# Kernel tuning notes

Measured on AMD Instinct MI355X. Metric: run time of the kernel, lower is better.

## Reference

```python
import jax, jax.numpy as jnp
import numpy as np

P = 8.0  # Lp exponent of the distance neuron (finite-p stage of l_inf-dist training)


def _patches(t, k, stride, pad):
    # [B, Cin, H, W] -> [B, Cin*k*k, H', W'], feature dim ordered channel-major
    return jax.lax.conv_general_dilated_patches(
        t, (k, k), (stride, stride), [(pad, pad), (pad, pad)])


def _lp(d):
    # d: [B, Cout, Cin*k*k, H', W'] nonnegative -> Lp norm over patch dim
    return jnp.power(jnp.sum(jnp.power(d, P), axis=2), 1.0 / P)


def norm_dist_conv(x, l, u, w, stride, pad):
    # Lp-distance "convolution": y[b,o,i,j] = || patch(x)[b,:,i,j] - w[o,:] ||_p
    # mean_normalize=True: zero-center each output unit's weight vector
    Cout, Cin, k, _ = w.shape
    wf = w.reshape(Cout, -1)
    wf = wf - jnp.mean(wf, axis=1, keepdims=True)
    wb = wf[None, :, :, None, None]                      # [1, Cout, Ckk, 1, 1]
    px = _patches(x, k, stride, pad)[:, None]            # [B, 1, Ckk, H', W']
    pl = _patches(l, k, stride, pad)[:, None]
    pu = _patches(u, k, stride, pad)[:, None]
    y = _lp(jnp.abs(px - wb))
    # interval bounds of |x_j - w_j| given x_j in [l_j, u_j], then monotone Lp
    dl = jnp.maximum(jnp.maximum(pl - wb, wb - pu), 0.0)
    du = jnp.maximum(jnp.abs(pl - wb), jnp.abs(pu - wb))
    return y, _lp(dl), _lp(du)


def bound_relu(x, l, u):
    # ReLU is monotone: apply elementwise to value and both bounds
    return jax.nn.relu(x), jax.nn.relu(l), jax.nn.relu(u)


def setup_inputs() -> dict:
    key = jax.random.key(0)
    k1, k2, k3 = jax.random.split(key, 3)
    B, C, H, W = 4, 32, 32, 32
    eps = 0.1  # l_inf perturbation radius
    x = jax.random.normal(k1, (B, C, H, W), dtype=jnp.float32)
    lower = x - eps
    upper = x + eps
    scale = 1.0 / np.sqrt(C * 9)
    weight1 = jax.random.normal(k2, (C, C, 3, 3), dtype=jnp.float32) * scale
    weight2 = jax.random.normal(k3, (C, C, 3, 3), dtype=jnp.float32) * scale
    return {"x": x, "lower": lower, "upper": upper,
            "weight1": weight1, "weight2": weight2}


def reference(x, lower, upper, weight1, weight2):
    # conv1 (stride=1, pad=1) -> BoundReLU -> conv2 -> residual add -> BoundReLU
    o = norm_dist_conv(x, lower, upper, weight1, 1, 1)
    o = bound_relu(*o)
    o = norm_dist_conv(*o, weight2, 1, 1)
    out = (o[0] + x, o[1] + lower, o[2] + upper)  # identity shortcut (stride=1, in==out)
    out = bound_relu(*out)
    return jnp.stack(out)  # [3, B, C, H, W]: (value, lower, upper)
```

## Files before the change

kernel.cpp:

```cpp
#include <hip/hip_runtime.h>

#define NB 4
#define NC 32
#define NH 32
#define NW 32
#define KK 288
#define PLANE (NB*NC*NH*NW)
#define CQ 8
#define SROW 36
#define SPL  (3*SROW)
#define SCH  (6*SPL)
#define STOT (CQ*SCH)

typedef float v2f __attribute__((ext_vector_type(2)));

__device__ __forceinline__ float s3(float v) { return sqrtf(sqrtf(sqrtf(v))); }
__device__ __forceinline__ v2f pkfma(v2f a, v2f b, v2f c) { return __builtin_elementwise_fma(a, b, c); }
__device__ __forceinline__ v2f pkmax(v2f a, v2f b) { return __builtin_elementwise_max(a, b); }

__global__ __launch_bounds__(256) void prep_weights_k(
        const float* __restrict__ w1, const float* __restrict__ w2,
        float* __restrict__ wf1, float* __restrict__ wf2)
{
    const int row = blockIdx.x;
    const float* src = (row < NC) ? w1 : w2;
    float* dst = (row < NC) ? wf1 : wf2;
    const int co = row & (NC - 1);
    const int tid = threadIdx.x;
    __shared__ float red[256];
    const float a = src[co*KK + tid];
    const float b = (tid + 256 < KK) ? src[co*KK + tid + 256] : 0.0f;
    red[tid] = a + b;
    __syncthreads();
    for (int s = 128; s > 0; s >>= 1) {
        if (tid < s) red[tid] += red[tid + s];
        __syncthreads();
    }
    const float mean = red[0] * (1.0f / (float)KK);
    const int q    = ((co >> 4) << 3) | (co & 7);
    const int slot = (co >> 3) & 1;
    {
        const int e = tid, c = e / 9, r9 = e - c*9, r = r9 / 3, kw = r9 - r*3;
        dst[((q*NC + c)*3 + r)*8 + kw*2 + slot] = a - mean;
    }
    if (tid + 256 < KK) {
        const int e = tid + 256, c = e / 9, r9 = e - c*9, r = r9 / 3, kw = r9 - r*3;
        dst[((q*NC + c)*3 + r)*8 + kw*2 + slot] = b - mean;
    }
}

template<bool STAGE2>
__global__ __launch_bounds__(256, 2) void normdist_conv_k(
    const float* __restrict__ sy,
    const float* __restrict__ sl,
    const float* __restrict__ su,
    const float* __restrict__ wf,
    float* __restrict__ pY, float* __restrict__ pL, float* __restrict__ pU)
{
    const int h4   = blockIdx.x;
    const int qg   = blockIdx.y >> 2;
    const int cq   = blockIdx.y & 3;
    const int cq0  = cq * CQ;
    const int b    = blockIdx.z;
    const int tid  = threadIdx.x;
    const int wv   = tid >> 6;
    const int lane = tid & 63;
    const int rsel = lane >> 4;
    const int pp   = lane & 15;
    const int p0   = pp * 2;

    __shared__ float sS[STOT];

    for (int i = tid; i < STOT; i += 256) {
        const int c   = i / SCH;
        int rem       = i - c*SCH;
        const int r   = rem / SPL;
        rem          -= r*SPL;
        const int pl  = rem / SROW;
        const int j   = rem - pl*SROW;
        const int gh  = 4*h4 + r - 1;
        const int gw  = j - 1;
        float v = 0.0f;
        if ((unsigned)gh < NH && (unsigned)gw < NW) {
            const int g = ((b*NC + cq0 + c)*NH + gh)*NW + gw;
            const float* s = (pl == 0) ? sy : (pl == 1) ? sl : su;
            if (STAGE2) {
                v = s3(s[g] + s[PLANE + g] + s[2*PLANE + g] + s[3*PLANE + g]);
            } else {
                v = s[g];
            }
        }
        sS[i] = v;
    }
    __syncthreads();

    const int q = qg*4 + wv;
    const float4* wq = (const float4*)wf + (q*NC + cq0)*6;
    const float* base = &sS[rsel*SPL + p0];

    v2f aY0 = {0,0}, aL0 = {0,0}, aU0 = {0,0};
    v2f aY1 = {0,0}, aL1 = {0,0}, aU1 = {0,0};

    auto tap2 = [&](v2f w, float pxv, float plv, float puv, v2f& aY, v2f& aL, v2f& aU) {
        const v2f P = {pxv, pxv};
        const v2f Lo = {plv, plv};
        const v2f Up = {puv, puv};
        const v2f d  = P - w;
        const v2f d2 = d*d, d4 = d2*d2;
        aY = pkfma(d4, d4, aY);
        const v2f a  = Lo - w;
        const v2f nb = w - Up;
        const v2f z  = {0.0f, 0.0f};
        const v2f m  = pkmax(pkmax(a, nb), z);
        const v2f m2 = m*m, m4 = m2*m2;
        aL = pkfma(m4, m4, aL);
        const v2f a2 = a*a, q2 = nb*nb;
        const v2f mm2 = pkmax(a2, q2);
        const v2f mm4 = mm2*mm2;
        aU = pkfma(mm4, mm4, aU);
    };

    float4 c0 = wq[0], c1 = wq[1], c2 = wq[2], c3 = wq[3], c4 = wq[4], c5 = wq[5];

    for (int c = 0; c < CQ; ++c) {
        const int cn = (c < CQ-1) ? c + 1 : c;
        const float4 n0 = wq[cn*6+0], n1 = wq[cn*6+1], n2 = wq[cn*6+2];
        const float4 n3 = wq[cn*6+3], n4 = wq[cn*6+4], n5 = wq[cn*6+5];

        const float* pb = base + c*SCH;
        #pragma unroll
        for (int dr = 0; dr < 3; ++dr) {
            const float* rb = pb + dr*SPL;
            const float X0 = rb[0],        X1 = rb[1],        X2 = rb[2],        X3 = rb[3];
            const float L0 = rb[SROW+0],   L1 = rb[SROW+1],   L2 = rb[SROW+2],   L3 = rb[SROW+3];
            const float U0 = rb[2*SROW+0], U1 = rb[2*SROW+1], U2 = rb[2*SROW+2], U3 = rb[2*SROW+3];

            const float4 wlo = (dr == 0) ? c0 : (dr == 1) ? c2 : c4;
            const float4 whi = (dr == 0) ? c1 : (dr == 1) ? c3 : c5;
            const v2f w0 = {wlo.x, wlo.y};
            const v2f w1 = {wlo.z, wlo.w};
            const v2f w2 = {whi.x, whi.y};

            tap2(w0, X0, L0, U0, aY0, aL0, aU0);
            tap2(w1, X1, L1, U1, aY0, aL0, aU0);
            tap2(w2, X2, L2, U2, aY0, aL0, aU0);
            tap2(w0, X1, L1, U1, aY1, aL1, aU1);
            tap2(w1, X2, L2, U2, aY1, aL1, aU1);
            tap2(w2, X3, L3, U3, aY1, aL1, aU1);
        }

        c0 = n0; c1 = n1; c2 = n2; c3 = n3; c4 = n4; c5 = n5;
    }

    const int co0 = ((q >> 3) << 4) | (q & 7);
    const int h   = 4*h4 + rsel;
    const int o   = ((b*NC + co0)*NH + h)*NW + p0;
    const int o1  = o + 8*NH*NW;

    float* dY = pY + cq*PLANE;
    float* dL = pL + cq*PLANE;
    float* dU = pU + cq*PLANE;
    *(float2*)&dY[o]  = make_float2(aY0.x, aY1.x);
    *(float2*)&dY[o1] = make_float2(aY0.y, aY1.y);
    *(float2*)&dL[o]  = make_float2(aL0.x, aL1.x);
    *(float2*)&dL[o1] = make_float2(aL0.y, aL1.y);
    *(float2*)&dU[o]  = make_float2(aU0.x, aU1.x);
    *(float2*)&dU[o1] = make_float2(aU0.y, aU1.y);
}

__global__ __launch_bounds__(256) void epilogue_k(
    const float* __restrict__ pY, const float* __restrict__ pL, const float* __restrict__ pU,
    const float* __restrict__ x,  const float* __restrict__ l,  const float* __restrict__ u,
    float* __restrict__ out)
{
    const int i = blockIdx.x*256 + threadIdx.x;
    const float4* pY4 = (const float4*)pY;
    const float4* pL4 = (const float4*)pL;
    const float4* pU4 = (const float4*)pU;
    const float4* x4  = (const float4*)x;
    const float4* l4  = (const float4*)l;
    const float4* u4  = (const float4*)u;
    float4* out4 = (float4*)out;
    const int Q = PLANE/4;

    const float4 ya = pY4[i], yb = pY4[Q+i], yc = pY4[2*Q+i], yd = pY4[3*Q+i];
    const float4 la = pL4[i], lb = pL4[Q+i], lc = pL4[2*Q+i], ld = pL4[3*Q+i];
    const float4 ua = pU4[i], ub = pU4[Q+i], uc = pU4[2*Q+i], ud = pU4[3*Q+i];
    const float4 xr = x4[i], lr = l4[i], ur = u4[i];

    float4 oy, ol, ou;
    oy.x = fmaxf(s3(ya.x+yb.x+yc.x+yd.x) + xr.x, 0.0f);
    oy.y = fmaxf(s3(ya.y+yb.y+yc.y+yd.y) + xr.y, 0.0f);
    oy.z = fmaxf(s3(ya.z+yb.z+yc.z+yd.z) + xr.z, 0.0f);
    oy.w = fmaxf(s3(ya.w+yb.w+yc.w+yd.w) + xr.w, 0.0f);
    ol.x = fmaxf(s3(la.x+lb.x+lc.x+ld.x) + lr.x, 0.0f);
    ol.y = fmaxf(s3(la.y+lb.y+lc.y+ld.y) + lr.y, 0.0f);
    ol.z = fmaxf(s3(la.z+lb.z+lc.z+ld.z) + lr.z, 0.0f);
    ol.w = fmaxf(s3(la.w+lb.w+lc.w+ld.w) + lr.w, 0.0f);
    ou.x = fmaxf(s3(ua.x+ub.x+uc.x+ud.x) + ur.x, 0.0f);
    ou.y = fmaxf(s3(ua.y+ub.y+uc.y+ud.y) + ur.y, 0.0f);
    ou.z = fmaxf(s3(ua.z+ub.z+uc.z+ud.z) + ur.z, 0.0f);
    ou.w = fmaxf(s3(ua.w+ub.w+uc.w+ud.w) + ur.w, 0.0f);

    out4[i]       = oy;
    out4[Q + i]   = ol;
    out4[2*Q + i] = ou;
}

extern "C" void kernel_launch(void* const* d_in, const int* in_sizes, int n_in,
                              void* d_out, int out_size, void* d_ws, size_t ws_size,
                              hipStream_t stream)
{
    const float* x  = (const float*)d_in[0];
    const float* l  = (const float*)d_in[1];
    const float* u  = (const float*)d_in[2];
    const float* w1 = (const float*)d_in[3];
    const float* w2 = (const float*)d_in[4];
    float* ws  = (float*)d_ws;
    float* wf1 = ws;
    float* wf2 = wf1 + 12288;
    float* p1Y = wf2 + 12288;
    float* p1L = p1Y + 4*PLANE;
    float* p1U = p1L + 4*PLANE;
    float* p2Y = p1U + 4*PLANE;
    float* p2L = p2Y + 4*PLANE;
    float* p2U = p2L + 4*PLANE;
    float* out = (float*)d_out;

    prep_weights_k<<<64, 256, 0, stream>>>(w1, w2, wf1, wf2);

    dim3 grd(NH/4, 16, NB);
    normdist_conv_k<false><<<grd, 256, 0, stream>>>(x, l, u, wf1, p1Y, p1L, p1U);
    normdist_conv_k<true ><<<grd, 256, 0, stream>>>(p1Y, p1L, p1U, wf2, p2Y, p2L, p2U);
    epilogue_k<<<PLANE/1024, 256, 0, stream>>>(p2Y, p2L, p2U, x, l, u, out);
}
```

Baseline: 115.0 us.

## Retile conv blocks to one row per block with interleaved float4 shared tile

Each block now covers a single output row and all 16 weight-pair groups for one channel quarter, instead of four rows and four weight groups. The shared tile stores x, lower and upper interleaved as float4, so each tap needs one LDS read instead of three. Input staging per block shrinks to three rows, halo overhead per output rises, and the register prefetch of the next channel's weights is dropped. Each lane now reads different weights (q depends on ps), so weight loads are less uniform across the wavefront.

```diff
diff --git a/kernel.cpp b/kernel.cpp
--- a/kernel.cpp
+++ b/kernel.cpp
@@ -7,10 +7,6 @@
 #define KK 288
 #define PLANE (NB*NC*NH*NW)
 #define CQ 8
-#define SROW 36
-#define SPL  (3*SROW)
-#define SCH  (6*SPL)
-#define STOT (CQ*SCH)
 
 typedef float v2f __attribute__((ext_vector_type(2)));
 
@@ -57,54 +53,51 @@
     const float* __restrict__ wf,
     float* __restrict__ pY, float* __restrict__ pL, float* __restrict__ pU)
 {
-    const int h4   = blockIdx.x;
-    const int qg   = blockIdx.y >> 2;
-    const int cq   = blockIdx.y & 3;
+    const int h    = blockIdx.x;
+    const int cq   = blockIdx.y;
     const int cq0  = cq * CQ;
     const int b    = blockIdx.z;
     const int tid  = threadIdx.x;
     const int wv   = tid >> 6;
     const int lane = tid & 63;
-    const int rsel = lane >> 4;
+    const int ps   = lane >> 4;
     const int pp   = lane & 15;
     const int p0   = pp * 2;
 
-    __shared__ float sS[STOT];
-
-    for (int i = tid; i < STOT; i += 256) {
-        const int c   = i / SCH;
-        int rem       = i - c*SCH;
-        const int r   = rem / SPL;
-        rem          -= r*SPL;
-        const int pl  = rem / SROW;
-        const int j   = rem - pl*SROW;
-        const int gh  = 4*h4 + r - 1;
-        const int gw  = j - 1;
-        float v = 0.0f;
+    __shared__ float4 sP[CQ*3*34];
+
+    for (int i = tid; i < CQ*3*34; i += 256) {
+        const int c   = i / 102;
+        const int rem = i - c*102;
+        const int r   = rem / 34;
+        const int col = rem - r*34;
+        const int gh  = h + r - 1;
+        const int gw  = col - 1;
+        float vx = 0.0f, vl = 0.0f, vu = 0.0f;
         if ((unsigned)gh < NH && (unsigned)gw < NW) {
             const int g = ((b*NC + cq0 + c)*NH + gh)*NW + gw;
-            const float* s = (pl == 0) ? sy : (pl == 1) ? sl : su;
             if (STAGE2) {
-                v = s3(s[g] + s[PLANE + g] + s[2*PLANE + g] + s[3*PLANE + g]);
+                vx = s3(sy[g] + sy[PLANE + g] + sy[2*PLANE + g] + sy[3*PLANE + g]);
+                vl = s3(sl[g] + sl[PLANE + g] + sl[2*PLANE + g] + sl[3*PLANE + g]);
+                vu = s3(su[g] + su[PLANE + g] + su[2*PLANE + g] + su[3*PLANE + g]);
             } else {
-                v = s[g];
+                vx = sy[g]; vl = sl[g]; vu = su[g];
             }
         }
-        sS[i] = v;
+        sP[i] = make_float4(vx, vl, vu, 0.0f);
     }
     __syncthreads();
 
-    const int q = qg*4 + wv;
+    const int q = wv*4 + ps;
     const float4* wq = (const float4*)wf + (q*NC + cq0)*6;
-    const float* base = &sS[rsel*SPL + p0];
 
     v2f aY0 = {0,0}, aL0 = {0,0}, aU0 = {0,0};
     v2f aY1 = {0,0}, aL1 = {0,0}, aU1 = {0,0};
 
-    auto tap2 = [&](v2f w, float pxv, float plv, float puv, v2f& aY, v2f& aL, v2f& aU) {
-        const v2f P = {pxv, pxv};
-        const v2f Lo = {plv, plv};
-        const v2f Up = {puv, puv};
+    auto tap2 = [&](v2f w, const float4& p, v2f& aY, v2f& aL, v2f& aU) {
+        const v2f P  = {p.x, p.x};
+        const v2f Lo = {p.y, p.y};
+        const v2f Up = {p.z, p.z};
         const v2f d  = P - w;
         const v2f d2 = d*d, d4 = d2*d2;
         aY = pkfma(d4, d4, aY);
@@ -120,40 +113,29 @@
         aU = pkfma(mm4, mm4, aU);
     };
 
-    float4 c0 = wq[0], c1 = wq[1], c2 = wq[2], c3 = wq[3], c4 = wq[4], c5 = wq[5];
-
     for (int c = 0; c < CQ; ++c) {
-        const int cn = (c < CQ-1) ? c + 1 : c;
-        const float4 n0 = wq[cn*6+0], n1 = wq[cn*6+1], n2 = wq[cn*6+2];
-        const float4 n3 = wq[cn*6+3], n4 = wq[cn*6+4], n5 = wq[cn*6+5];
-
-        const float* pb = base + c*SCH;
-        #pragma unroll
-        for (int dr = 0; dr < 3; ++dr) {
-            const float* rb = pb + dr*SPL;
-            const float X0 = rb[0],        X1 = rb[1],        X2 = rb[2],        X3 = rb[3];
-            const float L0 = rb[SROW+0],   L1 = rb[SROW+1],   L2 = rb[SROW+2],   L3 = rb[SROW+3];
-            const float U0 = rb[2*SROW+0], U1 = rb[2*SROW+1], U2 = rb[2*SROW+2], U3 = rb[2*SROW+3];
-
-            const float4 wlo = (dr == 0) ? c0 : (dr == 1) ? c2 : c4;
-            const float4 whi = (dr == 0) ? c1 : (dr == 1) ? c3 : c5;
-            const v2f w0 = {wlo.x, wlo.y};
-            const v2f w1 = {wlo.z, wlo.w};
-            const v2f w2 = {whi.x, whi.y};
-
-            tap2(w0, X0, L0, U0, aY0, aL0, aU0);
-            tap2(w1, X1, L1, U1, aY0, aL0, aU0);
-            tap2(w2, X2, L2, U2, aY0, aL0, aU0);
-            tap2(w0, X1, L1, U1, aY1, aL1, aU1);
-            tap2(w1, X2, L2, U2, aY1, aL1, aU1);
-            tap2(w2, X3, L3, U3, aY1, aL1, aU1);
-        }
-
-        c0 = n0; c1 = n1; c2 = n2; c3 = n3; c4 = n4; c5 = n5;
+        const int pb = c*102 + p0;
+        const float4 p00 = sP[pb +  0], p01 = sP[pb +  1], p02 = sP[pb +  2], p03 = sP[pb +  3];
+        const float4 p10 = sP[pb + 34], p11 = sP[pb + 35], p12 = sP[pb + 36], p13 = sP[pb + 37];
+        const float4 p20 = sP[pb + 68], p21 = sP[pb + 69], p22 = sP[pb + 70], p23 = sP[pb + 71];
+
+        const float4 w0lo = wq[c*6+0], w0hi = wq[c*6+1];
+        const float4 w1lo = wq[c*6+2], w1hi = wq[c*6+3];
+        const float4 w2lo = wq[c*6+4], w2hi = wq[c*6+5];
+
+        const v2f w00 = {w0lo.x, w0lo.y}, w01 = {w0lo.z, w0lo.w}, w02 = {w0hi.x, w0hi.y};
+        const v2f w10 = {w1lo.x, w1lo.y}, w11 = {w1lo.z, w1lo.w}, w12 = {w1hi.x, w1hi.y};
+        const v2f w20 = {w2lo.x, w2lo.y}, w21 = {w2lo.z, w2lo.w}, w22 = {w2hi.x, w2hi.y};
+
+        tap2(w00, p00, aY0, aL0, aU0); tap2(w01, p01, aY0, aL0, aU0); tap2(w02, p02, aY0, aL0, aU0);
+        tap2(w10, p10, aY0, aL0, aU0); tap2(w11, p11, aY0, aL0, aU0); tap2(w12, p12, aY0, aL0, aU0);
+        tap2(w20, p20, aY0, aL0, aU0); tap2(w21, p21, aY0, aL0, aU0); tap2(w22, p22, aY0, aL0, aU0);
+        tap2(w00, p01, aY1, aL1, aU1); tap2(w01, p02, aY1, aL1, aU1); tap2(w02, p03, aY1, aL1, aU1);
+        tap2(w10, p11, aY1, aL1, aU1); tap2(w11, p12, aY1, aL1, aU1); tap2(w12, p13, aY1, aL1, aU1);
+        tap2(w20, p21, aY1, aL1, aU1); tap2(w21, p22, aY1, aL1, aU1); tap2(w22, p23, aY1, aL1, aU1);
     }
 
     const int co0 = ((q >> 3) << 4) | (q & 7);
-    const int h   = 4*h4 + rsel;
     const int o   = ((b*NC + co0)*NH + h)*NW + p0;
     const int o1  = o + 8*NH*NW;
 
@@ -229,7 +211,7 @@
 
     prep_weights_k<<<64, 256, 0, stream>>>(w1, w2, wf1, wf2);
 
-    dim3 grd(NH/4, 16, NB);
+    dim3 grd(NH, 4, NB);
     normdist_conv_k<false><<<grd, 256, 0, stream>>>(x, l, u, wf1, p1Y, p1L, p1U);
     normdist_conv_k<true ><<<grd, 256, 0, stream>>>(p1Y, p1L, p1U, wf2, p2Y, p2L, p2U);
     epilogue_k<<<PLANE/1024, 256, 0, stream>>>(p2Y, p2L, p2U, x, l, u, out);
```

Result: faster. 103.3 us (-10.2%).
